# Optimization experiments

Hardware: AMD Instinct MI355X
Metric: run time of the kernel (lower is better)

## Reference

```python
import jax, jax.numpy as jnp
import numpy as np

B, S, H, V, NSPK = 8, 128, 768, 30000, 8


def gru_cell(x, h, wih, whh, bih, bhh):
    # torch GRU gate order: r, z, n
    gi = x @ wih.T + bih
    gh = h @ whh.T + bhh
    i_r, i_z, i_n = jnp.split(gi, 3, axis=-1)
    h_r, h_z, h_n = jnp.split(gh, 3, axis=-1)
    r = jax.nn.sigmoid(i_r + h_r)
    z = jax.nn.sigmoid(i_z + h_z)
    n = jnp.tanh(i_n + r * h_n)
    return (1.0 - z) * n + z * h


def setup_inputs() -> dict:
    key = jax.random.key(0)
    ks = jax.random.split(key, 32)
    nrm = lambda k, shp: (jax.random.normal(k, shp, dtype=jnp.float32) * 0.02)
    inp = {
        "chat_ids": jnp.arange(B, dtype=jnp.int32),
        "speaker_info": jax.random.randint(ks[0], (B, S), 0, NSPK),
        "sp_dialogues": jax.random.randint(ks[1], (B,), 0, NSPK),
        "sp_ind": jax.random.randint(ks[2], (B,), 0, NSPK),
        "inputs": jax.random.randint(ks[3], (B, S), 0, V),
        "emb": nrm(ks[4], (V, H)),
        # rnnD: GRU(E=H -> H)
        "d_wih": nrm(ks[5], (3 * H, H)), "d_whh": nrm(ks[6], (3 * H, H)),
        "d_bih": nrm(ks[7], (3 * H,)), "d_bhh": nrm(ks[8], (3 * H,)),
        # rnnG: GRU(3E -> H)
        "g_wih": nrm(ks[9], (3 * H, 3 * H)), "g_whh": nrm(ks[10], (3 * H, H)),
        "g_bih": nrm(ks[11], (3 * H,)), "g_bhh": nrm(ks[12], (3 * H,)),
        # rnnS: GRU(2E -> 2E)
        "s_wih": nrm(ks[13], (6 * H, 2 * H)), "s_whh": nrm(ks[14], (6 * H, 2 * H)),
        "s_bih": nrm(ks[15], (6 * H,)), "s_bhh": nrm(ks[16], (6 * H,)),
        # attention projections (qembed = kembed = hidden = E)
        "wq": nrm(ks[17], (H, H)), "bq": nrm(ks[18], (H,)),
        "wk": nrm(ks[19], (H, H)), "bk": nrm(ks[20], (H,)),
        "wv": nrm(ks[21], (H, H)), "bv": nrm(ks[22], (H,)),
        # fixed random initial states (torch.randn in forward)
        "h0": jax.random.normal(ks[23], (2 * H,), dtype=jnp.float32),
        "d_h0": jax.random.normal(ks[24], (H,), dtype=jnp.float32),
        "attn_h": jax.random.normal(ks[25], (H,), dtype=jnp.float32),
    }
    return inp


def _forward(chat_ids, speaker_info, inputs, emb,
             d_wih, d_whh, d_bih, d_bhh,
             g_wih, g_whh, g_bih, g_bhh,
             s_wih, s_whh, s_bih, s_bhh,
             wq, bq, wk, bk, wv, bv, h0, d_h0, attn_h):
    bert = emb[inputs]                              # [B,S,E]

    # rnnD over the whole dialogue (dropout is identity in eval)
    def d_step(h, x):
        h2 = gru_cell(x, h, d_wih, d_whh, d_bih, d_bhh)
        return h2, h2
    _, dlg = jax.lax.scan(d_step, jnp.zeros((B, H), bert.dtype), jnp.swapaxes(bert, 0, 1))
    dialogue = jnp.swapaxes(dlg, 0, 1)              # [B,S,H]

    speaker_seq = speaker_info[chat_ids]            # [B,S]
    scale = jnp.asarray(np.sqrt(H), dtype=dialogue.dtype)
    steps = jnp.arange(S)

    def batch_step(d_h, b_in):
        dlg_b, spk_b = b_in                         # [S,H], [S]
        op_buf0 = jnp.zeros((S, H), dialogue.dtype)
        sp0 = jnp.tile(h0[None, :], (NSPK, 1))      # every speaker starts at h0

        def step(carry, xs):
            op_buf, sp_states, dh = carry
            utt, spk, s = xs
            # growing-context attention over previously written op rows
            # (row s is still zero at this point, matching fop[b][:s+1])
            q = utt @ wq.T + bq                      # [H]
            K = op_buf @ wk.T + bk                   # [S,H]
            Vv = op_buf @ wv.T + bv                  # [S,H]
            scores = (K @ q) / scale                 # [S]
            mask = steps <= s
            probs = jax.nn.softmax(jnp.where(mask, scores, -jnp.inf))
            probs = jnp.where(jnp.isnan(probs), 0.0, probs)
            attn_out = probs @ Vv                    # [H]
            attn_part = jnp.where(s == 0, attn_h, attn_out)
            tmp = jnp.concatenate([attn_part, utt])  # [2H]
            h_spk = sp_states[spk]                   # dynamic speaker state
            h_new = gru_cell(tmp, h_spk, s_wih, s_whh, s_bih, s_bhh)
            spop_s = h_new + tmp                     # spop[b][s] = out + tmp
            sp_states = sp_states.at[spk].set(h_new)
            fop2_s = jnp.concatenate([spop_s, utt])  # [3H]
            op_s = gru_cell(fop2_s, dh, g_wih, g_whh, g_bih, g_bhh)
            op_buf = op_buf.at[s].set(op_s)
            return (op_buf, sp_states, op_s), (op_s, spop_s)

        (_, _, dh_out), (op_b, spop_b) = jax.lax.scan(
            step, (op_buf0, sp0, d_h), (dlg_b, spk_b, steps))
        return dh_out, (op_b, spop_b)

    # d_h carries across batch items, exactly as in the torch loop
    _, (op, spop) = jax.lax.scan(batch_step, d_h0, (dialogue, speaker_seq))
    return op, spop                                  # [B,S,H], [B,S,2H]


def reference(chat_ids, speaker_info, sp_dialogues, sp_ind, inputs, emb,
              d_wih, d_whh, d_bih, d_bhh,
              g_wih, g_whh, g_bih, g_bhh,
              s_wih, s_whh, s_bih, s_bhh,
              wq, bq, wk, bk, wv, bv, h0, d_h0, attn_h):
    return _forward(chat_ids, speaker_info, inputs, emb,
                    d_wih, d_whh, d_bih, d_bhh,
                    g_wih, g_whh, g_bih, g_bhh,
                    s_wih, s_whh, s_bih, s_bhh,
                    wq, bq, wk, bk, wv, bv, h0, d_h0, attn_h)
```

## Files before the change

kernel.cpp:

```cpp
#include <hip/hip_runtime.h>
#include <hip/hip_bf16.h>

typedef unsigned int uint32;
typedef unsigned short u16;
typedef unsigned long long u64;
typedef __attribute__((ext_vector_type(8))) short s16x8;
typedef __attribute__((ext_vector_type(4))) float f32x4;

#define H    768
#define H2   1536
#define H3   2304
#define H6   4608
#define BB   8
#define SS   128
#define GG   1024
#define NWG  256
#define NT   256
#define NTM  512
#define INVSCALE 0.036084391824351615f
#define SPIN_LIMIT (1 << 17)
#define DYN_LDS 163200

struct IN {
  const int *chat_ids, *speaker_info, *inputs;
  const float *emb, *d_wih, *d_whh, *d_bih, *d_bhh;
  const float *g_wih, *g_whh, *g_bih, *g_bhh;
  const float *s_wih, *s_whh, *s_bih, *s_bhh;
  const float *wq, *bq, *wk, *bk, *wv, *bv;
  const float *h0, *d_h0, *attn_h;
};

struct WS {
  int *flags1;
  float *Mqk, *Gsum;
  float *cu, *vkq, *cb, *cvs, *ch0s, *cvg, *chg0, *ghs0;
  float *Ms, *Mg;
  float *gi_d, *GIS;
  uint32 *gi_bf, *U_bf;
  float *dialogue, *U, *cvec, *GIG;
  float *gh_dbuf;
  float *sp_global;
  float *op_buf;
  u64 *op_tag;
  u64 *h_tag;
  u64 *sc_tag;
  float *probs_buf;
  float *h_buf, *Wbuf, *AO;
  float *out_op, *out_spop;
};

__device__ inline float sigm(float x) { return 1.f / (1.f + expf(-x)); }

__device__ inline u16 f2bf(float v) {
  __hip_bfloat16 b = __float2bfloat16(v);
  return *reinterpret_cast<u16*>(&b);
}
__device__ inline uint32 pack2bf(float a, float b) {
  return (uint32)f2bf(a) | ((uint32)f2bf(b) << 16);
}

__device__ inline float2 ld2(const float* p) { return *(const float2*)p; }
__device__ inline float2 ald2(const float* p) {
  u64 v = __hip_atomic_load((const u64*)p, __ATOMIC_RELAXED, __HIP_MEMORY_SCOPE_AGENT);
  union { u64 u; float2 f; } c; c.u = v; return c.f;
}
__device__ inline float ald(const float* p) {
  return __hip_atomic_load(p, __ATOMIC_RELAXED, __HIP_MEMORY_SCOPE_AGENT);
}
__device__ inline void ast(float* p, float v) {
  __hip_atomic_store(p, v, __ATOMIC_RELAXED, __HIP_MEMORY_SCOPE_AGENT);
}
__device__ inline void ast64(u64* p, u64 v) {
  __hip_atomic_store(p, v, __ATOMIC_RELAXED, __HIP_MEMORY_SCOPE_AGENT);
}
__device__ inline u64 ald64(const u64* p) {
  return __hip_atomic_load(p, __ATOMIC_RELAXED, __HIP_MEMORY_SCOPE_AGENT);
}
__device__ inline u64 tagf(int ep, float v) {
  return ((u64)(uint32)ep << 32) | (u64)__float_as_uint(v);
}

__device__ inline float pollf(const u64* p, int ep, int& bail) {
  int spins = 0;
  u64 v;
  for (;;) {
    v = ald64(p);
    if ((int)(v >> 32) >= ep) break;
    if (++spins > SPIN_LIMIT) { bail = 1; break; }
  }
  return __uint_as_float((uint32)v);
}

__device__ inline void gbar2(int* flags, int epoch, int& dead) {
  int bail = 0;
  __syncthreads();
  if (!dead) {
    if (threadIdx.x == 0)
      __hip_atomic_store(&flags[blockIdx.x * 16], epoch, __ATOMIC_RELAXED, __HIP_MEMORY_SCOPE_AGENT);
    if (threadIdx.x < NWG) {
      int spins = 0;
      while (__hip_atomic_load(&flags[threadIdx.x * 16], __ATOMIC_RELAXED, __HIP_MEMORY_SCOPE_AGENT) < epoch) {
        if (++spins > SPIN_LIMIT) { bail = 1; break; }
      }
    }
  }
  dead |= __syncthreads_or(bail);
  asm volatile("" ::: "memory");
}

template <int NI>
__device__ inline float dotr(const u16* wcol, const float2* xr) {
  const uint32* wp = (const uint32*)wcol;
  int l = threadIdx.x & 63;
  float acc = 0.f;
  #pragma unroll
  for (int i = 0; i < NI; i++) {
    uint32 u = wp[i * 64 + l];
    acc = fmaf(xr[i].x, __uint_as_float(u << 16),
          fmaf(xr[i].y, __uint_as_float(u & 0xffff0000u), acc));
  }
  #pragma unroll
  for (int o = 32; o > 0; o >>= 1) acc += __shfl_down(acc, o);
  return acc;
}
__device__ inline float xreduce(float a) {
  #pragma unroll
  for (int o = 32; o > 0; o >>= 1) a += __shfl_xor(a, o);
  return a;
}
template <int NI>
__device__ inline void loadx_lds(float2* xr, const float* x) {
  int l = threadIdx.x & 63;
  #pragma unroll
  for (int i = 0; i < NI; i++) xr[i] = ld2(x + 2 * (i * 64 + l));
}
template <int NI>
__device__ inline void loadx_atm(float2* xr, const float* x) {
  int l = threadIdx.x & 63;
  #pragma unroll
  for (int i = 0; i < NI; i++) xr[i] = ald2(x + 2 * (i * 64 + l));
}


__global__ __launch_bounds__(NT) void prep1_k(IN in, WS w) {
  long i = (long)blockIdx.x * NT + threadIdx.x;
  const long NG = (long)H3 * H;
  if (i < NG) {
    long n = i / H, k = i - n * H;
    w.Gsum[i] = in.g_wih[n * H3 + H + k] + in.g_wih[n * H3 + 2 * H + k];
  } else if (i < NG + H) {
    int m = (int)(i - NG);
    float a = 0.f;
    for (int t = 0; t < H; t++) a = fmaf(in.bq[t], in.wk[(long)t * H + m], a);
    w.cu[m] = a;
  } else if (i < NG + 2 * H) {
    int m = (int)(i - NG - H);
    float a = 0.f;
    for (int t = 0; t < H; t++) a = fmaf(in.bk[t], in.wq[(long)t * H + m], a);
    w.vkq[m] = a;
  } else if (i == NG + 2 * H) {
    float a = 0.f;
    for (int t = 0; t < H; t++) a = fmaf(in.bk[t], in.bq[t], a);
    w.cb[0] = a;
  }
}

__global__ __launch_bounds__(NT) void prep2_k(IN in, WS w) {
  int wid = blockIdx.x * (NT / 64) + (threadIdx.x >> 6);
  int l = threadIdx.x & 63;
  const int R1 = H6, R2 = H6 + H3, R3 = H6 + H3 + H6;
  if (wid < R1) {
    const float* row = in.s_wih + (long)wid * H2;
    float a = 0.f, c = 0.f;
    for (int i = l; i < H; i += 64) { float rv = row[i]; a = fmaf(in.bv[i], rv, a); c = fmaf(in.attn_h[i], rv, c); }
    #pragma unroll
    for (int o = 32; o > 0; o >>= 1) { a += __shfl_down(a, o); c += __shfl_down(c, o); }
    if (l == 0) { w.cvs[wid] = a; w.ch0s[wid] = c; }
  } else if (wid < R2) {
    int k = wid - R1;
    const float* row = in.g_wih + (long)k * H3;
    float a = 0.f, c = 0.f;
    for (int i = l; i < H; i += 64) { float rv = row[i]; a = fmaf(in.bv[i], rv, a); c = fmaf(in.attn_h[i], rv, c); }
    #pragma unroll
    for (int o = 32; o > 0; o >>= 1) { a += __shfl_down(a, o); c += __shfl_down(c, o); }
    if (l == 0) { w.cvg[k] = a; w.chg0[k] = c; }
  } else if (wid < R3) {
    int k = wid - R2;
    const float* row = in.s_whh + (long)k * H2;
    float a = 0.f;
    for (int i = l; i < H2; i += 64) a = fmaf(in.h0[i], row[i], a);
    #pragma unroll
    for (int o = 32; o > 0; o >>= 1) a += __shfl_down(a, o);
    if (l == 0) w.ghs0[k] = a + in.s_bhh[k];
  }
}

__global__ __launch_bounds__(NT) void pack_k(const float* src, uint32* dst, long n2) {
  long i = (long)blockIdx.x * NT + threadIdx.x;
  if (i < n2) dst[i] = pack2bf(src[2 * i], src[2 * i + 1]);
}

__global__ __launch_bounds__(NT) void gemm_k(const float* A, long sAm, long sAk,
                                             const float* B, long sBk,
                                             float* C, int M, int N, int K) {
  __shared__ float As[16][65];
  __shared__ float Bs[16][65];
  int m0 = blockIdx.y * 64, n0 = blockIdx.x * 64;
  int tid = threadIdx.x;
  int tx = tid & 15, ty = tid >> 4;
  float acc[4][4] = {};
  for (int k0 = 0; k0 < K; k0 += 16) {
    {
      int m = tid & 63, kb = tid >> 6;
      for (int p = 0; p < 4; p++) {
        int k = kb + p * 4;
        As[k][m] = A[(long)(m0 + m) * sAm + (long)(k0 + k) * sAk];
      }
    }
    {
      int n = tid & 63, kb = tid >> 6;
      for (int p = 0; p < 4; p++) {
        int k = kb + p * 4;
        Bs[k][n] = B[(long)(k0 + k) * sBk + (n0 + n)];
      }
    }
    __syncthreads();
    #pragma unroll
    for (int k = 0; k < 16; k++) {
      float a[4], b[4];
      #pragma unroll
      for (int i = 0; i < 4; i++) a[i] = As[k][ty * 4 + i];
      #pragma unroll
      for (int j = 0; j < 4; j++) b[j] = Bs[k][tx * 4 + j];
      #pragma unroll
      for (int i = 0; i < 4; i++)
        #pragma unroll
        for (int j = 0; j < 4; j++) acc[i][j] = fmaf(a[i], b[j], acc[i][j]);
    }
    __syncthreads();
  }
  for (int i = 0; i < 4; i++)
    for (int j = 0; j < 4; j++) {
      int m = m0 + ty * 4 + i, n = n0 + tx * 4 + j;
      C[(long)m * N + n] = acc[i][j];
    }
}

__global__ __launch_bounds__(NT) void mgemm_k(const float* A, long sAm, const int* gather,
                                              const float* B, long sB, int bColMajor,
                                              const float* bias, float* C, int N, int K) {
  __shared__ u16 Al[128 * 40];
  __shared__ u16 Bl[128 * 40];
  int tid = threadIdx.x;
  int n0 = blockIdx.x * 128, m0 = blockIdx.y * 128;
  int l = tid & 63, wv = tid >> 6;
  int wr = wv >> 1, wc = wv & 1;
  f32x4 acc[4][4] = {};
  long arow = gather ? (long)gather[m0 + (tid >> 1)] : (long)(m0 + (tid >> 1));
  for (int k0 = 0; k0 < K; k0 += 32) {
    __syncthreads();
    {
      int r = tid >> 1, half = tid & 1;
      const float* src = A + arow * sAm + k0 + half * 16;
      uint32* dst = (uint32*)(Al + r * 40 + half * 16);
      #pragma unroll
      for (int j = 0; j < 8; j++) dst[j] = pack2bf(src[2 * j], src[2 * j + 1]);
    }
    if (bColMajor) {
      int n = tid >> 1, half = tid & 1;
      const float* src = B + (long)(n0 + n) * sB + k0 + half * 16;
      uint32* dst = (uint32*)(Bl + n * 40 + half * 16);
      #pragma unroll
      for (int j = 0; j < 8; j++) dst[j] = pack2bf(src[2 * j], src[2 * j + 1]);
    } else {
      int kk = tid & 31, nb = tid >> 5;
      const float* src = B + (long)(k0 + kk) * sB + n0 + nb * 16;
      #pragma unroll
      for (int j = 0; j < 16; j++) Bl[(nb * 16 + j) * 40 + kk] = f2bf(src[j]);
    }
    __syncthreads();
    s16x8 af[4], bf[4];
    #pragma unroll
    for (int i = 0; i < 4; i++) {
      af[i] = *(const s16x8*)(Al + (wr * 64 + i * 16 + (l & 15)) * 40 + (l >> 4) * 8);
      bf[i] = *(const s16x8*)(Bl + (wc * 64 + i * 16 + (l & 15)) * 40 + (l >> 4) * 8);
    }
    #pragma unroll
    for (int i = 0; i < 4; i++)
      #pragma unroll
      for (int j = 0; j < 4; j++)
        acc[i][j] = __builtin_amdgcn_mfma_f32_16x16x32_bf16(af[i], bf[j], acc[i][j], 0, 0, 0);
  }
  #pragma unroll
  for (int i = 0; i < 4; i++)
    #pragma unroll
    for (int j = 0; j < 4; j++) {
      int n = n0 + wc * 64 + j * 16 + (l & 15);
      int mb = m0 + wr * 64 + i * 16 + ((l >> 4) << 2);
      float bb = bias ? bias[n] : 0.f;
      #pragma unroll
      for (int r = 0; r < 4; r++)
        C[(long)(mb + r) * N + n] = acc[i][j][r] + bb;
    }
}


__global__ __launch_bounds__(NTM) void coop_rnnD(IN in, WS w) {
  __shared__ u16 wD[9 * H];
  __shared__ float hB[BB][H];
  int tid = threadIdx.x, wg = blockIdx.x;
  int c0 = wg * 9;
  int l = tid & 63, wv = tid >> 6;
  for (int i = tid; i < 9 * H; i += NTM)
    wD[i] = f2bf(in.d_whh[(long)(c0 + i / H) * H + (i % H)]);
  __syncthreads();
  int epoch = 1, dead = 0;
  for (int t = 0; t < SS; t++) {
    if (t > 0) {
      float* ghb = w.gh_dbuf + (size_t)(t & 1) * BB * H3;
      for (int tk = wv; tk < 72; tk += 8) {
        int b = tk / 9, j = tk - b * 9;
        float2 xr[6];
        loadx_lds<6>(xr, hB[b]);
        float val = dotr<6>(wD + j * H, xr);
        if (l == 0) ast(ghb + (long)b * H3 + c0 + j, val + in.d_bhh[c0 + j]);
      }
      gbar2(w.flags1, epoch++, dead);
    }
    const float* ghb = w.gh_dbuf + (size_t)(t & 1) * BB * H3;
    for (int pc = tid; pc < BB * H / 2; pc += NTM) {
      int b = pc / (H / 2), k = 2 * (pc - b * (H / 2));
      const uint32* gi = w.gi_bf + ((long)(b * SS + t)) * (H3 / 2);
      uint32 u0 = gi[k >> 1], u1 = gi[(H + k) >> 1], u2 = gi[(2 * H + k) >> 1];
      float gr0 = __uint_as_float(u0 << 16), gr1 = __uint_as_float(u0 & 0xffff0000u);
      float gz0 = __uint_as_float(u1 << 16), gz1 = __uint_as_float(u1 & 0xffff0000u);
      float gn0 = __uint_as_float(u2 << 16), gn1 = __uint_as_float(u2 & 0xffff0000u);
      float hr0, hr1, hz0, hz1, hn0, hn1;
      if (t == 0) {
        hr0 = in.d_bhh[k]; hr1 = in.d_bhh[k + 1];
        hz0 = in.d_bhh[H + k]; hz1 = in.d_bhh[H + k + 1];
        hn0 = in.d_bhh[2 * H + k]; hn1 = in.d_bhh[2 * H + k + 1];
      } else {
        const float* gb = ghb + (long)b * H3;
        float2 a0 = ald2(gb + k), a1 = ald2(gb + H + k), a2 = ald2(gb + 2 * H + k);
        hr0 = a0.x; hr1 = a0.y; hz0 = a1.x; hz1 = a1.y; hn0 = a2.x; hn1 = a2.y;
      }
      float p0 = (t == 0) ? 0.f : hB[b][k], p1 = (t == 0) ? 0.f : hB[b][k + 1];
      float r0 = sigm(gr0 + hr0), r1 = sigm(gr1 + hr1);
      float z0 = sigm(gz0 + hz0), z1 = sigm(gz1 + hz1);
      float n0 = tanhf(gn0 + r0 * hn0), n1 = tanhf(gn1 + r1 * hn1);
      float h0v = (1.f - z0) * n0 + z0 * p0, h1v = (1.f - z1) * n1 + z1 * p1;
      hB[b][k] = h0v; hB[b][k + 1] = h1v;
      if (wg == 0) *(float2*)(w.dialogue + ((long)(b * SS + t)) * H + k) = make_float2(h0v, h1v);
    }
    __syncthreads();
  }
}

__global__ __launch_bounds__(NTM) void coop_main(IN in, WS w) {
  extern __shared__ char Lds[];
  u16*   wShh  = (u16*)(Lds + 0);
  u16*   wGab  = (u16*)(Lds + 55296);
  u16*   wMs   = (u16*)(Lds + 82944);
  u16*   wMg   = (u16*)(Lds + 110592);
  u16*   wGhh  = (u16*)(Lds + 124416);
  float* OPMSl = (float*)(Lds + 138240);
  float* OPMGl = (float*)(Lds + 147968);
  float* h_lds = (float*)(Lds + 152576);
  float* op_lds= (float*)(Lds + 158720);
  float* el    = (float*)(Lds + 161792);
  float* red   = (float*)(Lds + 162304);
  float* loc_si  = (float*)(Lds + 162560);
  float* loc_ghs = (float*)(Lds + 162632);
  float* loc_gw  = (float*)(Lds + 162776);
  float* loc_ghg = (float*)(Lds + 162812);
  float* loc_gih = (float*)(Lds + 162848);
  float* loc_gis = (float*)(Lds + 162884);
  float* loc_gig = (float*)(Lds + 162956);
  float* spc     = (float*)(Lds + 162992);

  int tid = threadIdx.x, wg = blockIdx.x;
  int l = tid & 63, wv = tid >> 6;
  int c0s = wg * 6, c0g3 = wg * 3;
  auto rrS = [&](int j) { return (j / 6) * H2 + c0s + (j % 6); };
  auto rrG = [&](int j) { return (j / 3) * H + c0g3 + (j % 3); };

  for (int i = tid; i < 18 * H2; i += NTM) { int j = i / H2, k = i - j * H2; wShh[i] = f2bf(in.s_whh[(long)rrS(j) * H2 + k]); }
  for (int i = tid; i < 9 * H2;  i += NTM) { int j = i / H2, k = i - j * H2; wGab[i] = f2bf(in.g_wih[(long)rrG(j) * H3 + k]); }
  for (int i = tid; i < 18 * H;  i += NTM) { int j = i / H,  k = i - j * H;  wMs[i]  = f2bf(w.Ms[(long)rrS(j) * H + k]); }
  for (int i = tid; i < 9 * H;   i += NTM) { int j = i / H,  k = i - j * H;  wMg[i]  = f2bf(w.Mg[(long)rrG(j) * H + k]); }
  for (int i = tid; i < 9 * H;   i += NTM) { int j = i / H,  k = i - j * H;  wGhh[i] = f2bf(in.g_whh[(long)rrG(j) * H + k]); }
  for (int i = tid; i < H; i += NTM) op_lds[i] = in.d_h0[i];
  __syncthreads();

  int dead = 0;

  for (int g = 0; g < GG; g++) {
    int s = g & 127, b = g >> 7;
    int g1 = g + 1, s1 = g1 & 127;
    int spk_cur = in.speaker_info[in.chat_ids[b] * SS + s];
    int spk_next = (g1 < GG) ? in.speaker_info[in.chat_ids[g1 >> 7] * SS + s1] : 0;
    float cv = w.cvec[g];
    if (tid < 18) loc_gis[tid] = w.GIS[(long)g * H6 + rrS(tid)];

    int bail = 0;
    if (!dead) {
      if (g > 0 && tid < 384) {
        int c = tid * 2;
        float v0 = pollf(w.op_tag + c, g, bail);
        float v1 = pollf(w.op_tag + c + 1, g, bail);
        op_lds[c] = v0; op_lds[c + 1] = v1;
      } else if (tid >= 384 && s >= 1) {
        int j = tid - 384;
        if (j <= s - 2)
          el[j] = expf(fminf(pollf(w.sc_tag + (size_t)(g & 1) * SS + j, g, bail), 30.f));
      }
    }
    dead |= __syncthreads_or(bail);

    if (s >= 1) {
      float2 xr[6];
      loadx_lds<6>(xr, op_lds);
      float a = 0.f;
      {
        const uint32* Ub = w.U_bf + (long)g * (H / 2);
        #pragma unroll
        for (int i = 0; i < 6; i++) {
          uint32 u = Ub[i * 64 + l];
          int idx = 2 * (i * 64 + l);
          a = fmaf(op_lds[idx], __uint_as_float(u << 16),
              fmaf(op_lds[idx + 1], __uint_as_float(u & 0xffff0000u), a));
        }
        a = xreduce(a);
      }
      float e1 = expf(fminf(a + cv, 30.f));
      float bs = 0.f;
      if (l <= s - 2) bs = el[l];
      if (l + 64 <= s - 2) bs += el[l + 64];
      bs = xreduce(bs);
      float suinv = 1.f / (e1 + bs + expf(fminf(cv, 30.f)));

      for (int r = wv; r < 36; r += 8) {
        if (r < 18) {
          float nr = dotr<6>(wMs + r * H, xr);
          float aa = 0.f;
          if (l <= s - 2) aa = el[l] * OPMSl[l * 19 + r];
          if (l + 64 <= s - 2) aa = fmaf(el[l + 64], OPMSl[(l + 64) * 19 + r], aa);
          #pragma unroll
          for (int o = 32; o > 0; o >>= 1) aa += __shfl_down(aa, o);
          if (l == 0) {
            OPMSl[(s - 1) * 19 + r] = nr;
            loc_si[r] = (aa + e1 * nr) * suinv + w.cvs[rrS(r)];
          }
        } else if (r < 27) {
          int t = r - 18;
          float nr = dotr<6>(wMg + t * H, xr);
          float aa = 0.f;
          if (l <= s - 2) aa = el[l] * OPMGl[l * 9 + t];
          if (l + 64 <= s - 2) aa = fmaf(el[l + 64], OPMGl[(l + 64) * 9 + t], aa);
          #pragma unroll
          for (int o = 32; o > 0; o >>= 1) aa += __shfl_down(aa, o);
          if (l == 0) {
            OPMGl[(s - 1) * 9 + t] = nr;
            loc_gw[t] = (aa + e1 * nr) * suinv + w.cvg[rrG(t)];
          }
        } else {
          int t = r - 27;
          float v = dotr<6>(wGhh + t * H, xr);
          if (l == 0) loc_ghg[t] = v + in.g_bhh[rrG(t)];
        }
      }
      if (g1 < GG && s1 != 0 && spk_next != spk_cur) {
        float2 xs[12];
        loadx_atm<12>(xs, w.sp_global + (long)spk_next * H2);
        for (int t = wv; t < 18; t += 8) {
          float v = dotr<12>(wShh + t * H2, xs);
          if (l == 0) loc_ghs[(g1 & 1) * 18 + t] = v + in.s_bhh[rrS(t)];
        }
      }
      if (wv == 7 && g1 < GG && s1 >= 2 && wg < s) {
        const float* opr = w.op_buf + (long)wg * H;
        const uint32* Ub1 = w.U_bf + (long)g1 * (H / 2);
        float a2 = 0.f;
        #pragma unroll
        for (int i0 = 0; i0 < 6; i0++) {
          int idx = i0 * 64 + l;
          float2 xa = ald2(opr + 2 * idx);
          uint32 u = Ub1[idx];
          a2 = fmaf(xa.x, __uint_as_float(u << 16),
               fmaf(xa.y, __uint_as_float(u & 0xffff0000u), a2));
        }
        #pragma unroll
        for (int o = 32; o > 0; o >>= 1) a2 += __shfl_down(a2, o);
        if (l == 0) ast64(w.sc_tag + (size_t)(g1 & 1) * SS + wg, tagf(g1, a2 + w.cvec[g1]));
      }
      if (wg == 0 && wv == 6) {
        int j = l;
        float pv = (j <= s - 2) ? el[j] * suinv : ((j == s - 1) ? e1 * suinv : 0.f);
        w.probs_buf[(long)g * SS + j] = pv;
        j = l + 64;
        pv = (j <= s - 2) ? el[j] * suinv : ((j == s - 1) ? e1 * suinv : 0.f);
        w.probs_buf[(long)g * SS + j] = pv;
      }
      __syncthreads();
    } else {
      if (tid < 18) loc_si[tid] = w.ch0s[rrS(tid)];
      else if (tid >= 32 && tid < 41) loc_gw[tid - 32] = w.chg0[rrG(tid - 32)];
      if (tid >= 64 && tid < 112) { int x = (tid - 64) / 6, t2 = (tid - 64) % 6; spc[x * 6 + t2] = in.h0[c0s + t2]; }
      if (tid >= 128 && tid < 176) {
        int x = (tid - 128) / 6, t2 = (tid - 128) % 6;
        if (x != spk_cur) ast(w.sp_global + (long)x * H2 + c0s + t2, in.h0[c0s + t2]);
      }
      if (wv == 3) {
        float2 xr[6];
        loadx_lds<6>(xr, op_lds);
        for (int j = 0; j < 9; j++) {
          float val = dotr<6>(wGhh + j * H, xr);
          if (l == 0) loc_ghg[j] = val + in.g_bhh[rrG(j)];
        }
      }
      if (wg == 0 && tid >= 384) w.probs_buf[(long)g * SS + (tid - 384)] = 0.f;
      __syncthreads();
    }

    float op_prev = (tid < 3) ? op_lds[c0g3 + tid] : 0.f;

    if (tid < 6) {
      int c = c0s + tid;
      float hprev = spc[spk_cur * 6 + tid];
      float ghr, ghz, ghn;
      if (s == 0) { ghr = w.ghs0[c]; ghz = w.ghs0[H2 + c]; ghn = w.ghs0[2 * H2 + c]; }
      else { const float* gb = loc_ghs + (g & 1) * 18; ghr = gb[tid]; ghz = gb[6 + tid]; ghn = gb[12 + tid]; }
      float gir = loc_gis[tid] + loc_si[tid];
      float giz = loc_gis[6 + tid] + loc_si[6 + tid];
      float gin = loc_gis[12 + tid] + loc_si[12 + tid];
      float r = sigm(gir + ghr), z = sigm(giz + ghz);
      float n = tanhf(gin + r * ghn);
      float hn = (1.f - z) * n + z * hprev;
      spc[spk_cur * 6 + tid] = hn;
      ast64(w.h_tag + c, tagf(g1, hn));
      ast(w.sp_global + (long)spk_cur * H2 + c, hn);
      w.h_buf[(long)g * H2 + c] = hn;
    }

    if (tid < 9) loc_gig[tid] = w.GIG[(long)g * H3 + rrG(tid)];
    bail = 0;
    if (!dead) {
      int c = tid * 3;
      float v0 = pollf(w.h_tag + c, g1, bail);
      float v1 = pollf(w.h_tag + c + 1, g1, bail);
      float v2 = pollf(w.h_tag + c + 2, g1, bail);
      h_lds[c] = v0; h_lds[c + 1] = v1; h_lds[c + 2] = v2;
    }
    dead |= __syncthreads_or(bail);

    {
      int needsh = (g1 < GG && s1 != 0 && (spk_next == spk_cur || s == 0)) ? 1 : 0;
      int diff = (spk_next != spk_cur);
      if (needsh) {
        float2 xs[12];
        if (diff) loadx_atm<12>(xs, w.sp_global + (long)spk_next * H2);
        else loadx_lds<12>(xs, h_lds);
        for (int t = wv; t < 18; t += 8) {
          float val = dotr<12>(wShh + t * H2, xs);
          if (l == 0) loc_ghs[(g1 & 1) * 18 + t] = val + in.s_bhh[rrS(t)];
        }
      }
      {
        float2 xh[12];
        loadx_lds<12>(xh, h_lds);
        for (int t = wv; t < 9; t += 8) {
          float val = dotr<12>(wGab + t * H2, xh);
          if (l == 0) loc_gih[t] = val;
        }
      }
    }
    __syncthreads();

    if (tid < 3) {
      int c = c0g3 + tid;
      float gir = loc_gig[tid]     + loc_gw[tid]     + loc_gih[tid];
      float giz = loc_gig[3 + tid] + loc_gw[3 + tid] + loc_gih[3 + tid];
      float gin = loc_gig[6 + tid] + loc_gw[6 + tid] + loc_gih[6 + tid];
      float r = sigm(gir + loc_ghg[tid]);
      float z = sigm(giz + loc_ghg[3 + tid]);
      float n = tanhf(gin + r * loc_ghg[6 + tid]);
      float o = (1.f - z) * n + z * op_prev;
      ast(w.op_buf + (long)s * H + c, o);
      w.out_op[(long)g * H + c] = o;
      asm volatile("s_waitcnt vmcnt(0)" ::: "memory");
      ast64(w.op_tag + c, tagf(g1, o));
    }
  }
}


__global__ __launch_bounds__(NT) void fixup_u_k(WS w) {
  long i = (long)blockIdx.x * NT + threadIdx.x;
  if (i < (long)GG * H) {
    int m = (int)(i % H);
    w.U[i] = (w.U[i] + w.cu[m]) * INVSCALE;
  }
}

__global__ __launch_bounds__(NT) void cvec_k(WS w) {
  int g = blockIdx.x * 4 + (threadIdx.x >> 6);
  int l = threadIdx.x & 63;
  const float* d = w.dialogue + (long)g * H;
  float p = 0.f;
  for (int i = l; i < H; i += 64) p = fmaf(d[i], w.vkq[i], p);
  #pragma unroll
  for (int o = 32; o > 0; o >>= 1) p += __shfl_down(p, o);
  if (l == 0) w.cvec[g] = (p + w.cb[0]) * INVSCALE;
}

__global__ __launch_bounds__(NT) void epi_W_k(WS w) {
  int g = blockIdx.x, b = g >> 7;
  __shared__ float pl[SS];
  if (threadIdx.x < SS) pl[threadIdx.x] = w.probs_buf[(long)g * SS + threadIdx.x];
  __syncthreads();
  const float* opb = w.out_op + (long)b * SS * H;
  for (int n = threadIdx.x; n < H; n += NT) {
    float acc = 0.f;
    for (int j = 0; j < SS; j++) acc = fmaf(pl[j], opb[(long)j * H + n], acc);
    w.Wbuf[(long)g * H + n] = acc;
  }
}

__global__ __launch_bounds__(NT) void assemble_k(IN in, WS w) {
  long idx = (long)blockIdx.x * NT + threadIdx.x;
  if (idx >= (long)GG * H2) return;
  long g = idx / H2;
  int k = (int)(idx - g * H2);
  int s = (int)(g & 127);
  float t;
  if (k < H) t = (s == 0) ? in.attn_h[k] : w.AO[g * H + k];
  else t = w.dialogue[g * H + (k - H)];
  w.out_spop[idx] = w.h_buf[idx] + t;
}


extern "C" void kernel_launch(void* const* d_in, const int* in_sizes, int n_in,
                              void* d_out, int out_size, void* d_ws, size_t ws_size,
                              hipStream_t stream) {
  IN in;
  in.chat_ids = (const int*)d_in[0];
  in.speaker_info = (const int*)d_in[1];
  in.inputs = (const int*)d_in[4];
  in.emb = (const float*)d_in[5];
  in.d_wih = (const float*)d_in[6];  in.d_whh = (const float*)d_in[7];
  in.d_bih = (const float*)d_in[8];  in.d_bhh = (const float*)d_in[9];
  in.g_wih = (const float*)d_in[10]; in.g_whh = (const float*)d_in[11];
  in.g_bih = (const float*)d_in[12]; in.g_bhh = (const float*)d_in[13];
  in.s_wih = (const float*)d_in[14]; in.s_whh = (const float*)d_in[15];
  in.s_bih = (const float*)d_in[16]; in.s_bhh = (const float*)d_in[17];
  in.wq = (const float*)d_in[18];  in.bq = (const float*)d_in[19];
  in.wk = (const float*)d_in[20];  in.bk = (const float*)d_in[21];
  in.wv = (const float*)d_in[22];  in.bv = (const float*)d_in[23];
  in.h0 = (const float*)d_in[24];  in.d_h0 = (const float*)d_in[25];
  in.attn_h = (const float*)d_in[26];

  char* base = (char*)d_ws;
  size_t off = 0;
  auto A = [&](size_t bytes) -> void* {
    size_t r = (off + 255) & ~(size_t)255;
    off = r + bytes;
    return (void*)(base + r);
  };
  WS w;
  w.flags1 = (int*)A(NWG * 16 * 4);
  w.Mqk = (float*)A((size_t)H * H * 4);
  w.Gsum = (float*)A((size_t)H3 * H * 4);
  w.cu = (float*)A(H * 4);
  w.vkq = (float*)A(H * 4);
  w.cb = (float*)A(4);
  w.cvs = (float*)A(H6 * 4);
  w.ch0s = (float*)A(H6 * 4);
  w.cvg = (float*)A(H3 * 4);
  w.chg0 = (float*)A(H3 * 4);
  w.ghs0 = (float*)A(H6 * 4);
  w.Ms = (float*)A((size_t)H6 * H * 4);
  w.Mg = (float*)A((size_t)H3 * H * 4);
  {
    void* r1 = A((size_t)GG * H6 * 4);
    w.gi_d = (float*)r1;
    w.GIS = (float*)r1;
  }
  w.gi_bf = (uint32*)A((size_t)GG * H3 * 2);
  w.U_bf = (uint32*)A((size_t)GG * H * 2);
  w.dialogue = (float*)A((size_t)GG * H * 4);
  w.U = (float*)A((size_t)GG * H * 4);
  w.cvec = (float*)A(GG * 4);
  w.GIG = (float*)A((size_t)GG * H3 * 4);
  w.gh_dbuf = (float*)A((size_t)2 * BB * H3 * 4);
  w.sp_global = (float*)A((size_t)BB * H2 * 4);
  w.op_buf = (float*)A((size_t)SS * H * 4);
  w.op_tag = (u64*)A((size_t)H * 8);
  w.h_tag = (u64*)A((size_t)H2 * 8);
  w.sc_tag = (u64*)A((size_t)2 * SS * 8);
  w.probs_buf = (float*)A((size_t)GG * SS * 4);
  w.h_buf = (float*)A((size_t)GG * H2 * 4);
  w.Wbuf = (float*)A((size_t)GG * H * 4);
  w.AO = (float*)A((size_t)GG * H * 4);
  w.out_op = (float*)d_out;
  w.out_spop = (float*)d_out + (size_t)GG * H;

  (void)hipFuncSetAttribute((const void*)coop_main, hipFuncAttributeMaxDynamicSharedMemorySize, DYN_LDS);

  (void)hipMemsetAsync(w.flags1, 0, NWG * 16 * 4, stream);
  (void)hipMemsetAsync(w.op_tag, 0, (size_t)H * 8, stream);
  (void)hipMemsetAsync(w.h_tag, 0, (size_t)H2 * 8, stream);
  (void)hipMemsetAsync(w.sc_tag, 0, (size_t)2 * SS * 8, stream);

  const long NG = (long)H3 * H;
  prep1_k<<<(int)((NG + 2 * H + 1 + NT - 1) / NT), NT, 0, stream>>>(in, w);
  prep2_k<<<(H6 + H3 + H6 + 3) / 4, NT, 0, stream>>>(in, w);

  gemm_k<<<dim3(H / 64, H / 64), NT, 0, stream>>>(in.wq, 1, H, in.wk, H, w.Mqk, H, H, H);
  mgemm_k<<<dim3(H / 128, H6 / 128), NT, 0, stream>>>(in.s_wih, H2, nullptr, in.wv, H, 0, nullptr, w.Ms, H, H);
  mgemm_k<<<dim3(H / 128, H3 / 128), NT, 0, stream>>>(in.g_wih, H3, nullptr, in.wv, H, 0, nullptr, w.Mg, H, H);
  mgemm_k<<<dim3(H3 / 128, GG / 128), NT, 0, stream>>>(in.emb, H, in.inputs, in.d_wih, H, 1, in.d_bih, w.gi_d, H3, H);
  pack_k<<<(int)(((long)GG * H3 / 2 + NT - 1) / NT), NT, 0, stream>>>(w.gi_d, w.gi_bf, (long)GG * H3 / 2);
  coop_rnnD<<<NWG, NTM, 0, stream>>>(in, w);

  mgemm_k<<<dim3(H / 128, GG / 128), NT, 0, stream>>>(w.dialogue, H, nullptr, w.Mqk, H, 0, nullptr, w.U, H, H);
  mgemm_k<<<dim3(H6 / 128, GG / 128), NT, 0, stream>>>(w.dialogue, H, nullptr, in.s_wih + H, H2, 1, in.s_bih, w.GIS, H6, H);
  mgemm_k<<<dim3(H3 / 128, GG / 128), NT, 0, stream>>>(w.dialogue, H, nullptr, w.Gsum, H, 1, in.g_bih, w.GIG, H3, H);
  fixup_u_k<<<(GG * H + NT - 1) / NT, NT, 0, stream>>>(w);
  pack_k<<<(int)(((long)GG * H / 2 + NT - 1) / NT), NT, 0, stream>>>(w.U, w.U_bf, (long)GG * H / 2);
  cvec_k<<<GG / 4, NT, 0, stream>>>(w);

  coop_main<<<NWG, NTM, DYN_LDS, stream>>>(in, w);

  epi_W_k<<<GG, NT, 0, stream>>>(w);
  mgemm_k<<<dim3(H / 128, GG / 128), NT, 0, stream>>>(w.Wbuf, H, nullptr, in.wv, H, 1, in.bv, w.AO, H, H);
  assemble_k<<<(int)(((long)GG * H2 + NT - 1) / NT), NT, 0, stream>>>(in, w);
}
```

Measured before the change: 14.85 ms.

## Pack three bf16 values per tagged word and fuse gate dot into one wave

Changes the inter-workgroup handoff so each 64-bit tagged word carries a 16-bit epoch plus three bf16 values. That cuts the number of polled words per step for op and h exchange by a factor of three. Wave 0 now computes the G-input dot products itself and immediately does the rnnG cell update, keeping op state in registers. This removes a __syncthreads and the LDS round trip, while the other waves handle the S hidden-hidden dots. The cost is bf16 precision on the values exchanged between workgroups, which feed later steps and can lower accuracy.

```diff
diff --git a/kernel.cpp b/kernel.cpp
--- a/kernel.cpp
+++ b/kernel.cpp
@@ -58,6 +58,7 @@
 __device__ inline uint32 pack2bf(float a, float b) {
   return (uint32)f2bf(a) | ((uint32)f2bf(b) << 16);
 }
+__device__ inline float bf2f(uint32 u) { return __uint_as_float(u << 16); }
 
 __device__ inline float2 ld2(const float* p) { return *(const float2*)p; }
 __device__ inline float2 ald2(const float* p) {
@@ -78,6 +79,9 @@
 }
 __device__ inline u64 tagf(int ep, float v) {
   return ((u64)(uint32)ep << 32) | (u64)__float_as_uint(v);
+}
+__device__ inline u64 tag3(int ep, float a, float b, float c) {
+  return ((u64)(uint32)ep << 48) | ((u64)f2bf(c) << 32) | ((u64)f2bf(b) << 16) | (u64)f2bf(a);
 }
 
 __device__ inline float pollf(const u64* p, int ep, int& bail) {
@@ -89,6 +93,16 @@
     if (++spins > SPIN_LIMIT) { bail = 1; break; }
   }
   return __uint_as_float((uint32)v);
+}
+__device__ inline u64 poll48(const u64* p, int ep, int& bail) {
+  int spins = 0;
+  u64 v;
+  for (;;) {
+    v = ald64(p);
+    if ((int)(v >> 48) >= ep) break;
+    if (++spins > SPIN_LIMIT) { bail = 1; break; }
+  }
+  return v;
 }
 
 __device__ inline void gbar2(int* flags, int epoch, int& dead) {
@@ -394,6 +408,10 @@
   __syncthreads();
 
   int dead = 0;
+  float opw[3];
+  if (wv == 0 && l == 0) {
+    opw[0] = in.d_h0[c0g3]; opw[1] = in.d_h0[c0g3 + 1]; opw[2] = in.d_h0[c0g3 + 2];
+  }
 
   for (int g = 0; g < GG; g++) {
     int s = g & 127, b = g >> 7;
@@ -405,11 +423,11 @@
 
     int bail = 0;
     if (!dead) {
-      if (g > 0 && tid < 384) {
-        int c = tid * 2;
-        float v0 = pollf(w.op_tag + c, g, bail);
-        float v1 = pollf(w.op_tag + c + 1, g, bail);
-        op_lds[c] = v0; op_lds[c + 1] = v1;
+      if (g > 0 && tid < 256) {
+        u64 v = poll48(w.op_tag + tid, g, bail);
+        op_lds[3 * tid]     = bf2f((uint32)(v & 0xffffu));
+        op_lds[3 * tid + 1] = bf2f((uint32)((v >> 16) & 0xffffu));
+        op_lds[3 * tid + 2] = bf2f((uint32)((v >> 32) & 0xffffu));
       } else if (tid >= 384 && s >= 1) {
         int j = tid - 384;
         if (j <= s - 2)
@@ -523,8 +541,7 @@
       __syncthreads();
     }
 
-    float op_prev = (tid < 3) ? op_lds[c0g3 + tid] : 0.f;
-
+    float hn_val = 0.f;
     if (tid < 6) {
       int c = c0s + tid;
       float hprev = spc[spk_cur * 6 + tid];
@@ -538,58 +555,61 @@
       float n = tanhf(gin + r * ghn);
       float hn = (1.f - z) * n + z * hprev;
       spc[spk_cur * 6 + tid] = hn;
-      ast64(w.h_tag + c, tagf(g1, hn));
       ast(w.sp_global + (long)spk_cur * H2 + c, hn);
       w.h_buf[(long)g * H2 + c] = hn;
+      hn_val = hn;
+    }
+    if (wv == 0) {
+      float p0 = __shfl(hn_val, 0), p1 = __shfl(hn_val, 1), p2 = __shfl(hn_val, 2);
+      float p3 = __shfl(hn_val, 3), p4 = __shfl(hn_val, 4), p5 = __shfl(hn_val, 5);
+      if (l == 0) ast64(w.h_tag + 2 * wg, tag3(g1, p0, p1, p2));
+      else if (l == 1) ast64(w.h_tag + 2 * wg + 1, tag3(g1, p3, p4, p5));
     }
 
     if (tid < 9) loc_gig[tid] = w.GIG[(long)g * H3 + rrG(tid)];
     bail = 0;
     if (!dead) {
-      int c = tid * 3;
-      float v0 = pollf(w.h_tag + c, g1, bail);
-      float v1 = pollf(w.h_tag + c + 1, g1, bail);
-      float v2 = pollf(w.h_tag + c + 2, g1, bail);
-      h_lds[c] = v0; h_lds[c + 1] = v1; h_lds[c + 2] = v2;
+      u64 v = poll48(w.h_tag + tid, g1, bail);
+      h_lds[3 * tid]     = bf2f((uint32)(v & 0xffffu));
+      h_lds[3 * tid + 1] = bf2f((uint32)((v >> 16) & 0xffffu));
+      h_lds[3 * tid + 2] = bf2f((uint32)((v >> 32) & 0xffffu));
     }
     dead |= __syncthreads_or(bail);
 
-    {
+    if (wv == 0) {
+      float2 xh[12];
+      loadx_lds<12>(xh, h_lds);
+      float gih[9];
+      #pragma unroll
+      for (int j = 0; j < 9; j++) gih[j] = dotr<12>(wGab + j * H2, xh);
+      if (l == 0) {
+        #pragma unroll
+        for (int t = 0; t < 3; t++) {
+          float gir = loc_gig[t]     + loc_gw[t]     + gih[t];
+          float giz = loc_gig[3 + t] + loc_gw[3 + t] + gih[3 + t];
+          float gin = loc_gig[6 + t] + loc_gw[6 + t] + gih[6 + t];
+          float r = sigm(gir + loc_ghg[t]);
+          float z = sigm(giz + loc_ghg[3 + t]);
+          float n = tanhf(gin + r * loc_ghg[6 + t]);
+          float o = (1.f - z) * n + z * opw[t];
+          opw[t] = o;
+          ast(w.op_buf + (long)s * H + c0g3 + t, o);
+          w.out_op[(long)g * H + c0g3 + t] = o;
+        }
+      }
+      asm volatile("s_waitcnt vmcnt(0)" ::: "memory");
+      if (l == 0) ast64(w.op_tag + wg, tag3(g1, opw[0], opw[1], opw[2]));
+    } else {
       int needsh = (g1 < GG && s1 != 0 && (spk_next == spk_cur || s == 0)) ? 1 : 0;
-      int diff = (spk_next != spk_cur);
       if (needsh) {
         float2 xs[12];
-        if (diff) loadx_atm<12>(xs, w.sp_global + (long)spk_next * H2);
+        if (spk_next != spk_cur) loadx_atm<12>(xs, w.sp_global + (long)spk_next * H2);
         else loadx_lds<12>(xs, h_lds);
-        for (int t = wv; t < 18; t += 8) {
-          float val = dotr<12>(wShh + t * H2, xs);
-          if (l == 0) loc_ghs[(g1 & 1) * 18 + t] = val + in.s_bhh[rrS(t)];
+        for (int r = wv - 1; r < 18; r += 7) {
+          float val = dotr<12>(wShh + r * H2, xs);
+          if (l == 0) loc_ghs[(g1 & 1) * 18 + r] = val + in.s_bhh[rrS(r)];
         }
       }
-      {
-        float2 xh[12];
-        loadx_lds<12>(xh, h_lds);
-        for (int t = wv; t < 9; t += 8) {
-          float val = dotr<12>(wGab + t * H2, xh);
-          if (l == 0) loc_gih[t] = val;
-        }
-      }
-    }
-    __syncthreads();
-
-    if (tid < 3) {
-      int c = c0g3 + tid;
-      float gir = loc_gig[tid]     + loc_gw[tid]     + loc_gih[tid];
-      float giz = loc_gig[3 + tid] + loc_gw[3 + tid] + loc_gih[3 + tid];
-      float gin = loc_gig[6 + tid] + loc_gw[6 + tid] + loc_gih[6 + tid];
-      float r = sigm(gir + loc_ghg[tid]);
-      float z = sigm(giz + loc_ghg[3 + tid]);
-      float n = tanhf(gin + r * loc_ghg[6 + tid]);
-      float o = (1.f - z) * n + z * op_prev;
-      ast(w.op_buf + (long)s * H + c, o);
-      w.out_op[(long)g * H + c] = o;
-      asm volatile("s_waitcnt vmcnt(0)" ::: "memory");
-      ast64(w.op_tag + c, tagf(g1, o));
     }
   }
 }
@@ -695,8 +715,8 @@
   w.gh_dbuf = (float*)A((size_t)2 * BB * H3 * 4);
   w.sp_global = (float*)A((size_t)BB * H2 * 4);
   w.op_buf = (float*)A((size_t)SS * H * 4);
-  w.op_tag = (u64*)A((size_t)H * 8);
-  w.h_tag = (u64*)A((size_t)H2 * 8);
+  w.op_tag = (u64*)A((size_t)NWG * 8);
+  w.h_tag = (u64*)A((size_t)2 * NWG * 8);
   w.sc_tag = (u64*)A((size_t)2 * SS * 8);
   w.probs_buf = (float*)A((size_t)GG * SS * 4);
   w.h_buf = (float*)A((size_t)GG * H2 * 4);
@@ -708,8 +728,8 @@
   (void)hipFuncSetAttribute((const void*)coop_main, hipFuncAttributeMaxDynamicSharedMemorySize, DYN_LDS);
 
   (void)hipMemsetAsync(w.flags1, 0, NWG * 16 * 4, stream);
-  (void)hipMemsetAsync(w.op_tag, 0, (size_t)H * 8, stream);
-  (void)hipMemsetAsync(w.h_tag, 0, (size_t)H2 * 8, stream);
+  (void)hipMemsetAsync(w.op_tag, 0, (size_t)NWG * 8, stream);
+  (void)hipMemsetAsync(w.h_tag, 0, (size_t)2 * NWG * 8, stream);
   (void)hipMemsetAsync(w.sc_tag, 0, (size_t)2 * SS * 8, stream);
 
   const long NG = (long)H3 * H;
```

After: 17.49 ms. 17.8% more time.
